# Kernel optimization log

Measured on AMD Instinct MI355X. Metric: run time of the kernel, lower is better.

The kernel has to match this reference:

```python
import jax, jax.numpy as jnp
import numpy as np

N, E, C, L, NG = 50000, 600000, 128, 7, 512
EPS = 1e-7


def layer_norm(z, g, b):
    mu = z.mean(-1, keepdims=True)
    var = ((z - mu) ** 2).mean(-1, keepdims=True)
    return (z - mu) * jax.lax.rsqrt(var + 1e-5) * g + b


def setup_inputs() -> dict:
    key = jax.random.key(0)
    ks = jax.random.split(key, 16)
    inp = {
        'x': jax.random.randint(ks[0], (N, 9), 0, 64, dtype=jnp.int32),
        'edge_index': jax.random.randint(ks[1], (2, E), 0, N, dtype=jnp.int32),
        'edge_attr': jax.random.randint(ks[2], (E, 3), 0, 8, dtype=jnp.int32),
        'batch': jnp.sort(jax.random.randint(ks[3], (N,), 0, NG, dtype=jnp.int32)),
        'atom_emb': jax.random.normal(ks[4], (9, 64, C), jnp.float32) * 0.1,
        'bond_emb': jax.random.normal(ks[5], (3, 8, C), jnp.float32) * 0.1,
        'vn_emb': jnp.zeros((1, C), jnp.float32),
        'conv_W1': jax.random.normal(ks[6], (L, C, 2 * C), jnp.float32) / np.sqrt(C),
        'conv_b1': jnp.zeros((L, 2 * C), jnp.float32),
        'conv_g1': jnp.ones((L, 2 * C), jnp.float32),
        'conv_bb1': jnp.zeros((L, 2 * C), jnp.float32),
        'conv_W2': jax.random.normal(ks[7], (L, 2 * C, C), jnp.float32) / np.sqrt(2 * C),
        'conv_b2': jnp.zeros((L, C), jnp.float32),
        'norm_g': jnp.ones((L, C), jnp.float32),
        'norm_b': jnp.zeros((L, C), jnp.float32),
        'vn_W1': jax.random.normal(ks[8], (L - 1, C, C), jnp.float32) / np.sqrt(C),
        'vn_b1': jnp.zeros((L - 1, C), jnp.float32),
        'vn_g': jnp.ones((L - 1, C), jnp.float32),
        'vn_bb': jnp.zeros((L - 1, C), jnp.float32),
        'vn_W2': jax.random.normal(ks[9], (L - 1, C, C), jnp.float32) / np.sqrt(C),
        'vn_b2': jnp.zeros((L - 1, C), jnp.float32),
    }
    return inp


def reference(x, edge_index, edge_attr, batch, atom_emb, bond_emb, vn_emb,
              conv_W1, conv_b1, conv_g1, conv_bb1, conv_W2, conv_b2,
              norm_g, norm_b, vn_W1, vn_b1, vn_g, vn_bb, vn_W2, vn_b2):
    src, dst = edge_index[0], edge_index[1]

    # AtomEncoder: sum of per-feature embeddings -> [N, C]
    h = atom_emb[jnp.arange(9), x].sum(axis=1)
    # BondEncoder (conv_encode_edge=False) -> [E, C]
    edge_emb = bond_emb[jnp.arange(3), edge_attr].sum(axis=1)

    # virtual node embedding (one per graph)
    vn = jnp.broadcast_to(vn_emb[0], (NG, C))
    h = h + vn[batch]

    def gen_conv(l, hx):
        # GENConv: msg = relu(x_j + e) + eps; softmax aggregation (t=1); MLP(x+m)
        msg = jax.nn.relu(hx[src] + edge_emb) + EPS                      # [E, C]
        mx = jax.ops.segment_max(msg, dst, num_segments=N)               # [N, C]
        e = jnp.exp(msg - mx[dst])
        den = jax.ops.segment_sum(e, dst, num_segments=N)
        m = jax.ops.segment_sum(msg * (e / (den[dst] + 1e-16)), dst, num_segments=N)
        z = hx + m
        z = jax.nn.relu(layer_norm(z @ conv_W1[l] + conv_b1[l], conv_g1[l], conv_bb1[l]))
        return z @ conv_W2[l] + conv_b2[l]

    # res+ block: Conv -> [Norm -> ReLU -> (VN update) -> Conv + res]*
    h = gen_conv(0, h)
    for l in range(1, L):
        h2 = jax.nn.relu(layer_norm(h, norm_g[l - 1], norm_b[l - 1]))
        vtmp = jax.ops.segment_sum(h2, batch, num_segments=NG) + vn
        v = jax.nn.relu(layer_norm(vtmp @ vn_W1[l - 1] + vn_b1[l - 1], vn_g[l - 1], vn_bb[l - 1]))
        vn = v @ vn_W2[l - 1] + vn_b2[l - 1]
        h2 = h2 + vn[batch]
        h = gen_conv(l, h2) + h
    h = layer_norm(h, norm_g[L - 1], norm_b[L - 1])

    # global_add_pool -> [NG, C]
    return jax.ops.segment_sum(h, batch, num_segments=NG)
```

## Files before the change

kernel.cpp:

```cpp
#include <hip/hip_runtime.h>
#include <hip/hip_bf16.h>
#include <stdint.h>

#define N_NODES 50000
#define N_EDGES 600000
#define CH 128
#define NLAYERS 7
#define NGRAPHS 512

typedef __hip_bfloat16 bf16;
using bf16x8 = __attribute__((ext_vector_type(8))) __bf16;
using f32x4  = __attribute__((ext_vector_type(4))) float;
using u32x4  = __attribute__((ext_vector_type(4))) uint32_t;

static __device__ __forceinline__ float b2f(bf16 v){ return __bfloat162float(v); }

static __device__ __forceinline__ void bar_lds(){
  asm volatile("s_waitcnt lgkmcnt(0)" ::: "memory");
  __builtin_amdgcn_sched_barrier(0);
  __builtin_amdgcn_s_barrier();
}

__global__ void k_detect(const uint32_t* __restrict__ g, int* __restrict__ flag){
  if (threadIdx.x == 0 && blockIdx.x == 0) flag[0] = (g[0] == 0x3F803F80u) ? 1 : 0;
}

struct Segs { const void* src[12]; float* dst[12]; int n[12]; };

__global__ void k_cvt_all(const int* __restrict__ flag, Segs S){
  int f = flag[0];
  int seg = blockIdx.y;
  int n = S.n[seg];
  const void* src = S.src[seg];
  float* dst = S.dst[seg];
  for (int i = blockIdx.x*blockDim.x + threadIdx.x; i < n; i += gridDim.x*blockDim.x)
    dst[i] = f ? b2f(((const bf16*)src)[i]) : ((const float*)src)[i];
}

__global__ void k_transpose_all(const int* __restrict__ flag,
    const void* W1, const void* W2, const void* vW1, const void* vW2,
    bf16* W1p, bf16* W2T, bf16* vW1p, bf16* vW2T){
  int f = flag[0];
  const int T0 = NLAYERS*128*256, T1 = NLAYERS*256*128;
  const int T2 = (NLAYERS-1)*128*128;
  int total = T0+T1+2*T2;
  for (int i = blockIdx.x*blockDim.x + threadIdx.x; i < total; i += gridDim.x*blockDim.x){
    float v;
    if (i < T0){
      int idx = i; int l = idx/(128*256); int rem = idx - l*128*256; int k = rem >> 8; int n = rem & 255;
      v = f ? b2f(((const bf16*)W1)[idx]) : ((const float*)W1)[idx];
      W1p[(size_t)l*256*128 + n*128 + (k ^ ((n&7)<<3))] = __float2bfloat16(v);
    } else if (i < T0+T1){
      int idx = i-T0; int l = idx/(256*128); int rem = idx - l*256*128; int k = rem >> 7; int n = rem & 127;
      v = f ? b2f(((const bf16*)W2)[idx]) : ((const float*)W2)[idx];
      W2T[(size_t)l*128*256 + n*256 + k] = __float2bfloat16(v);
    } else if (i < T0+T1+T2){
      int idx = i-T0-T1; int l = idx/(128*128); int rem = idx - l*128*128; int k = rem >> 7; int n = rem & 127;
      v = f ? b2f(((const bf16*)vW1)[idx]) : ((const float*)vW1)[idx];
      vW1p[(size_t)l*128*128 + n*128 + (k ^ ((n&7)<<3))] = __float2bfloat16(v);
    } else {
      int idx = i-T0-T1-T2; int l = idx/(128*128); int rem = idx - l*128*128; int k = rem >> 7; int n = rem & 127;
      v = f ? b2f(((const bf16*)vW2)[idx]) : ((const float*)vW2)[idx];
      vW2T[(size_t)l*128*128 + n*128 + k] = __float2bfloat16(v);
    }
  }
}

__global__ void k_bondC(const int* __restrict__ flag, const void* __restrict__ bond,
                        float* __restrict__ bondC){
  int f = flag[0];
  int i = blockIdx.x*blockDim.x + threadIdx.x;
  if (i >= 512*128) return;
  int idx = i >> 7, c = i & 127;
  int a0 = idx & 7, a1 = (idx>>3) & 7, a2 = (idx>>6) & 7;
  auto g = [&](int e)->float{ return f ? b2f(((const bf16*)bond)[e]) : ((const float*)bond)[e]; };
  bondC[i] = g((0*8+a0)*128 + c) + g((1*8+a1)*128 + c) + g((2*8+a2)*128 + c);
}

__global__ void k_zero_i32(int* p, int n){
  for (int i = blockIdx.x*blockDim.x + threadIdx.x; i < n; i += gridDim.x*blockDim.x) p[i] = 0;
}

__global__ void k_hist(const int* __restrict__ keys, int* __restrict__ counts, int n){
  for (int i = blockIdx.x*blockDim.x + threadIdx.x; i < n; i += gridDim.x*blockDim.x)
    atomicAdd(&counts[keys[i]], 1);
}

__global__ __launch_bounds__(256) void k_scanA(const int* __restrict__ in, int* __restrict__ out,
                                               int* __restrict__ bsums, int n){
  __shared__ int lds[256];
  int t = threadIdx.x;
  int base = blockIdx.x * 1024;
  int v[4]; int s = 0;
  #pragma unroll
  for (int i=0;i<4;i++){ int idx = base + t*4 + i; int x = (idx<n)? in[idx] : 0; v[i]=x; s+=x; }
  lds[t] = s; __syncthreads();
  for (int off=1; off<256; off<<=1){
    int x = (t>=off)? lds[t-off] : 0;
    __syncthreads();
    lds[t] += x;
    __syncthreads();
  }
  int p = lds[t] - s;
  #pragma unroll
  for (int i=0;i<4;i++){ int idx = base + t*4 + i; if (idx<n) out[idx] = p; p += v[i]; }
  if (t==255) bsums[blockIdx.x] = lds[255];
}

__global__ __launch_bounds__(256) void k_scanB(int* bsums, int nblk){
  __shared__ int lds[256];
  int t = threadIdx.x;
  int v = (t<nblk)? bsums[t] : 0;
  lds[t] = v; __syncthreads();
  for (int off=1; off<256; off<<=1){
    int x = (t>=off)? lds[t-off] : 0;
    __syncthreads();
    lds[t] += x;
    __syncthreads();
  }
  if (t<nblk) bsums[t] = lds[t] - v;
}

__global__ void k_scanC(int* out, const int* bsums, int n){
  for (int i = blockIdx.x*blockDim.x + threadIdx.x; i < n; i += gridDim.x*blockDim.x)
    out[i] += bsums[i >> 10];
}

__global__ void k_scatter(const int* __restrict__ ei, const int* __restrict__ ea,
                          const int* __restrict__ row_ptr, int* __restrict__ fill,
                          uint32_t* __restrict__ csr){
  for (int e = blockIdx.x*blockDim.x + threadIdx.x; e < N_EDGES; e += gridDim.x*blockDim.x){
    int src = ei[e];
    int dst = ei[N_EDGES + e];
    int pos = row_ptr[dst] + atomicAdd(&fill[dst], 1);
    uint32_t a0 = (uint32_t)ea[e*3+0], a1 = (uint32_t)ea[e*3+1], a2 = (uint32_t)ea[e*3+2];
    csr[pos] = (uint32_t)src | ((a0 | (a1<<3) | (a2<<6)) << 16);
  }
}

__global__ void k_gptr(const int* __restrict__ batch, int* __restrict__ gptr){
  int i = blockIdx.x*blockDim.x + threadIdx.x;
  if (i >= N_NODES) return;
  int b = batch[i];
  if (i == 0){ for (int g=0; g<=b; ++g) gptr[g] = 0; }
  else { int bp = batch[i-1]; for (int g=bp+1; g<=b; ++g) gptr[g] = i; }
  if (i == N_NODES-1){ for (int g=b+1; g<=NGRAPHS; ++g) gptr[g] = N_NODES; }
}

__global__ __launch_bounds__(128) void k_atom_encode(const int* __restrict__ x,
    const float* __restrict__ atom_emb, const float* __restrict__ vn_emb,
    uint32_t* __restrict__ hxb){
  int n = blockIdx.x; int c = threadIdx.x;
  float s = vn_emb[c];
  #pragma unroll
  for (int f=0; f<9; ++f){
    int xv = x[n*9+f];
    s += atom_emb[(f*64 + xv)*CH + c];
  }
  float o = __shfl_xor(s, 1);
  if ((c & 1) == 0){
    __hip_bfloat162 p; p.x = __float2bfloat16(s); p.y = __float2bfloat16(o);
    hxb[n*64 + (c>>1)] = *reinterpret_cast<uint32_t*>(&p);
  }
}

__global__ void k_vn_init(const float* __restrict__ vn_emb, float* __restrict__ vn){
  for (int i = blockIdx.x*blockDim.x + threadIdx.x; i < NGRAPHS*CH; i += gridDim.x*blockDim.x)
    vn[i] = vn_emb[i & (CH-1)];
}

__global__ __launch_bounds__(64) void k_aggregate(const uint32_t* __restrict__ hxb,
     const uint32_t* __restrict__ csr, const int* __restrict__ row_ptr,
     const float* __restrict__ bondC, uint32_t* __restrict__ z){
  int n = blockIdx.x; int t = threadIdx.x;
  int s0 = row_ptr[n], s1 = row_ptr[n+1];
  float sa=0.f, sb=0.f, wa=0.f, wb=0.f;
  int i = s0;
  for (; i+4 <= s1; i += 4){
    uint32_t u0=csr[i], u1=csr[i+1], u2=csr[i+2], u3=csr[i+3];
    uint32_t h0 = hxb[(size_t)(u0 & 0xFFFFu)*64 + t];
    uint32_t h1 = hxb[(size_t)(u1 & 0xFFFFu)*64 + t];
    uint32_t h2 = hxb[(size_t)(u2 & 0xFFFFu)*64 + t];
    uint32_t h3 = hxb[(size_t)(u3 & 0xFFFFu)*64 + t];
    float2 c0 = *reinterpret_cast<const float2*>(bondC + (size_t)(u0 >> 16)*128 + 2*t);
    float2 c1 = *reinterpret_cast<const float2*>(bondC + (size_t)(u1 >> 16)*128 + 2*t);
    float2 c2 = *reinterpret_cast<const float2*>(bondC + (size_t)(u2 >> 16)*128 + 2*t);
    float2 c3 = *reinterpret_cast<const float2*>(bondC + (size_t)(u3 >> 16)*128 + 2*t);
    #define EDGE(hp, bc) { \
      float va = __uint_as_float(hp << 16) + bc.x; \
      float vb = __uint_as_float(hp & 0xFFFF0000u) + bc.y; \
      va = fmaxf(va, 0.f) + 1e-7f; vb = fmaxf(vb, 0.f) + 1e-7f; \
      float pa = __expf(va - 10.f), pb = __expf(vb - 10.f); \
      sa += pa; wa += pa*va; sb += pb; wb += pb*vb; }
    EDGE(h0, c0) EDGE(h1, c1) EDGE(h2, c2) EDGE(h3, c3)
  }
  for (; i < s1; ++i){
    uint32_t u = csr[i];
    uint32_t hp = hxb[(size_t)(u & 0xFFFFu)*64 + t];
    float2 bc = *reinterpret_cast<const float2*>(bondC + (size_t)(u >> 16)*128 + 2*t);
    EDGE(hp, bc)
    #undef EDGE
  }
  uint32_t own = hxb[(size_t)n*64 + t];
  float za = __uint_as_float(own << 16)         + wa/(sa + 1e-16f);
  float zb = __uint_as_float(own & 0xFFFF0000u) + wb/(sb + 1e-16f);
  __hip_bfloat162 p; p.x = __float2bfloat16(za); p.y = __float2bfloat16(zb);
  z[(size_t)n*64 + (t ^ ((n&7)<<2))] = *reinterpret_cast<uint32_t*>(&p);
}

template<int K, int N1, int N2, bool VNIN>
__global__ __launch_bounds__(512, 2) void k_mlp7(const bf16* __restrict__ A,
    const float* __restrict__ Af32,
    const bf16* __restrict__ W1s,
    const float* __restrict__ b1, const float* __restrict__ g1, const float* __restrict__ bb1,
    const bf16* __restrict__ W2T,
    const float* __restrict__ b2,
    const float* __restrict__ lng, const float* __restrict__ lnb,
    const float* __restrict__ residual, float* __restrict__ out,
    float* __restrict__ hxout, int relu2, int M, int NT)
{
  constexpr int KK1 = K/32;
  constexpr int WC  = N1/4;
  constexpr int JC  = WC/16;
  constexpr int KK2 = N1/32;
  __shared__ __align__(16) bf16 W1L[N1*K];
  __shared__ __align__(16) bf16 AL[2][64*K];
  __shared__ __align__(16) bf16 zt[64*N1];
  __shared__ float lnp[64][4][2];
  __shared__ float lnv[64][2];

  const int tid = threadIdx.x;
  const int wid = tid >> 6, lane = tid & 63;
  const int wr = wid >> 2, wc = wid & 3;
  const int rlo = lane & 15, hi = lane >> 4, khi = hi*8;

  {
    constexpr int NC_ = (N1*K*2)/1024/8;
    #pragma unroll
    for (int c=0;c<NC_;++c){
      int cc = c*8 + wid;
      __builtin_amdgcn_global_load_lds((const uint32_t*)((const char*)W1s + cc*1024 + lane*16),
                                       (uint32_t*)((char*)W1L + cc*1024), 16, 0, 0);
    }
  }

  float b1v[JC], gv[JC], bbv[JC];
  #pragma unroll
  for (int jc=0;jc<JC;++jc){
    int col = wc*WC + jc*16 + rlo;
    b1v[jc] = b1[col]; gv[jc] = g1[col]; bbv[jc] = bb1[col];
  }
  float bv2[2] = { b2[wc*32 + rlo], b2[wc*32 + 16 + rlo] };
  float lngv[2] = {0.f,0.f}, lnbv[2] = {0.f,0.f};
  if (hxout){
    lngv[0] = lng[wc*32 + rlo];      lnbv[0] = lnb[wc*32 + rlo];
    lngv[1] = lng[wc*32 + 16 + rlo]; lnbv[1] = lnb[wc*32 + 16 + rlo];
  }
  u32x4 b2raw[2][KK2];
  #pragma unroll
  for (int ct=0;ct<2;++ct){
    const bf16* wp = W2T + (size_t)(wc*32 + ct*16 + rlo)*N1 + khi;
    #pragma unroll
    for (int kk=0;kk<KK2;++kk){
      b2raw[ct][kk] = *reinterpret_cast<const u32x4*>(wp + kk*32);
      asm volatile("" : "+v"(b2raw[ct][kk]));
    }
  }

  auto stageA = [&](int nb, int tile){
    if constexpr (!VNIN){
      const char* src = (const char*)A + (size_t)tile*(64*K*2);
      constexpr int NCA = (64*K*2)/1024/8;
      #pragma unroll
      for (int c=0;c<NCA;++c){
        int cc = c*8 + wid;
        __builtin_amdgcn_global_load_lds((const uint32_t*)(src + cc*1024 + lane*16),
                                         (uint32_t*)((char*)&AL[nb][0] + cc*1024), 16, 0, 0);
      }
    } else {
      int base = tile*64;
      #pragma unroll
      for (int e=0;e<(64*K/4)/512;++e){
        int idx = tid + e*512;
        int row = idx >> 5;
        int k4  = (idx & 31)*4;
        float4 v = *reinterpret_cast<const float4*>(Af32 + (size_t)(base+row)*K + k4);
        int s = (row&7)<<3;
        bf16* d = &AL[nb][row*K + (k4 ^ s)];
        d[0]=__float2bfloat16(v.x); d[1]=__float2bfloat16(v.y);
        d[2]=__float2bfloat16(v.z); d[3]=__float2bfloat16(v.w);
      }
    }
  };

  int t = blockIdx.x, buf = 0;
  stageA(0, t);
  __syncthreads();

  while (true){
    int tn = t + (int)gridDim.x;

    f32x4 acc1[2][JC];
    #pragma unroll
    for (int rt=0;rt<2;++rt)
      #pragma unroll
      for (int jc=0;jc<JC;++jc) acc1[rt][jc] = {0.f,0.f,0.f,0.f};
    #pragma unroll
    for (int kk=0;kk<KK1;++kk){
      bf16x8 af[2], bw[JC];
      #pragma unroll
      for (int rt=0;rt<2;++rt){
        int lr = wr*32 + rt*16 + rlo;
        af[rt] = *reinterpret_cast<const bf16x8*>(&AL[buf][lr*K + ((kk*32 + khi) ^ ((lr&7)<<3))]);
      }
      #pragma unroll
      for (int jc=0;jc<JC;++jc){
        int n = wc*WC + jc*16 + rlo;
        bw[jc] = *reinterpret_cast<const bf16x8*>(&W1L[n*K + ((kk*32 + khi) ^ ((n&7)<<3))]);
      }
      #pragma unroll
      for (int rt=0;rt<2;++rt)
        #pragma unroll
        for (int jc=0;jc<JC;++jc)
          acc1[rt][jc] = __builtin_amdgcn_mfma_f32_16x16x32_bf16(af[rt], bw[jc], acc1[rt][jc], 0,0,0);
    }

    if (tn < NT) stageA(buf^1, tn);
    float resv[2][2][4];
    if (residual){
      #pragma unroll
      for (int rt=0;rt<2;++rt)
        #pragma unroll
        for (int r=0;r<4;++r){
          int grow = t*64 + wr*32 + rt*16 + hi*4 + r; if (grow >= M) grow = M-1;
          #pragma unroll
          for (int ct=0;ct<2;++ct)
            resv[rt][ct][r] = residual[(size_t)grow*N2 + wc*32 + ct*16 + rlo];
        }
    }
    __builtin_amdgcn_sched_barrier(0);

    float p[2][4], q[2][4];
    #pragma unroll
    for (int rt=0;rt<2;++rt)
      #pragma unroll
      for (int r=0;r<4;++r){ p[rt][r]=0.f; q[rt][r]=0.f; }
    #pragma unroll
    for (int jc=0;jc<JC;++jc)
      #pragma unroll
      for (int rt=0;rt<2;++rt)
        #pragma unroll
        for (int r=0;r<4;++r){
          float v = acc1[rt][jc][r] + b1v[jc]; acc1[rt][jc][r] = v;
          p[rt][r] += v; q[rt][r] += v*v;
        }
    #pragma unroll
    for (int rt=0;rt<2;++rt)
      #pragma unroll
      for (int r=0;r<4;++r){
        float pv = p[rt][r], qv = q[rt][r];
        #pragma unroll
        for (int off=1; off<16; off<<=1){ pv += __shfl_xor(pv, off); qv += __shfl_xor(qv, off); }
        if (rlo == 0){
          int row = wr*32 + rt*16 + hi*4 + r;
          lnp[row][wc][0] = pv; lnp[row][wc][1] = qv;
        }
      }
    bar_lds();
    if (tid < 64){
      float P=0.f, Q=0.f;
      #pragma unroll
      for (int w=0;w<4;++w){ P += lnp[tid][w][0]; Q += lnp[tid][w][1]; }
      float mu = P*(1.f/N1);
      lnv[tid][0] = mu;
      lnv[tid][1] = rsqrtf(Q*(1.f/N1) - mu*mu + 1e-5f);
    }
    bar_lds();

    #pragma unroll
    for (int rt=0;rt<2;++rt)
      #pragma unroll
      for (int r=0;r<4;++r){
        int row = wr*32 + rt*16 + hi*4 + r;
        float mu = lnv[row][0], rs = lnv[row][1];
        #pragma unroll
        for (int jc=0;jc<JC;++jc){
          int col = wc*WC + jc*16 + rlo;
          float y = (acc1[rt][jc][r]-mu)*rs*gv[jc] + bbv[jc];
          zt[row*N1 + (col ^ ((row&7)<<3))] = __float2bfloat16(fmaxf(y, 0.f));
        }
      }
    bar_lds();

    f32x4 acc2[2][2];
    #pragma unroll
    for (int rt=0;rt<2;++rt)
      #pragma unroll
      for (int ct=0;ct<2;++ct) acc2[rt][ct] = {0.f,0.f,0.f,0.f};
    #pragma unroll
    for (int kk=0;kk<KK2;++kk){
      bf16x8 a2[2];
      #pragma unroll
      for (int rt=0;rt<2;++rt){
        int row = wr*32 + rt*16 + rlo;
        a2[rt] = *reinterpret_cast<const bf16x8*>(&zt[row*N1 + ((kk*32 + khi) ^ ((row&7)<<3))]);
      }
      #pragma unroll
      for (int rt=0;rt<2;++rt)
        #pragma unroll
        for (int ct=0;ct<2;++ct){
          bf16x8 bb;
          __builtin_memcpy(&bb, &b2raw[ct][kk], 16);
          acc2[rt][ct] = __builtin_amdgcn_mfma_f32_16x16x32_bf16(a2[rt], bb, acc2[rt][ct], 0,0,0);
        }
    }

    float vmat[2][2][4];
    #pragma unroll
    for (int rt=0;rt<2;++rt)
      #pragma unroll
      for (int ct=0;ct<2;++ct)
        #pragma unroll
        for (int r=0;r<4;++r){
          float v = acc2[rt][ct][r] + bv2[ct];
          if (residual) v += resv[rt][ct][r];
          vmat[rt][ct][r] = v;
          int grow = t*64 + wr*32 + rt*16 + hi*4 + r;
          if (grow < M) out[(size_t)grow*N2 + wc*32 + ct*16 + rlo] = v;
        }

    if (hxout){
      #pragma unroll
      for (int rt=0;rt<2;++rt)
        #pragma unroll
        for (int r=0;r<4;++r){
          float pv = vmat[rt][0][r] + vmat[rt][1][r];
          float qv = vmat[rt][0][r]*vmat[rt][0][r] + vmat[rt][1][r]*vmat[rt][1][r];
          #pragma unroll
          for (int off=1; off<16; off<<=1){ pv += __shfl_xor(pv, off); qv += __shfl_xor(qv, off); }
          if (rlo == 0){
            int row = wr*32 + rt*16 + hi*4 + r;
            lnp[row][wc][0] = pv; lnp[row][wc][1] = qv;
          }
        }
      bar_lds();
      if (tid < 64){
        float P=0.f, Q=0.f;
        #pragma unroll
        for (int w=0;w<4;++w){ P += lnp[tid][w][0]; Q += lnp[tid][w][1]; }
        float mu = P*(1.f/N2);
        lnv[tid][0] = mu;
        lnv[tid][1] = rsqrtf(Q*(1.f/N2) - mu*mu + 1e-5f);
      }
      bar_lds();
      #pragma unroll
      for (int rt=0;rt<2;++rt)
        #pragma unroll
        for (int r=0;r<4;++r){
          int row = wr*32 + rt*16 + hi*4 + r;
          float mu = lnv[row][0], rs = lnv[row][1];
          int grow = t*64 + row;
          if (grow < M){
            #pragma unroll
            for (int ct=0;ct<2;++ct){
              float y = (vmat[rt][ct][r]-mu)*rs*lngv[ct] + lnbv[ct];
              if (relu2) y = fmaxf(y, 0.f);
              hxout[(size_t)grow*N2 + wc*32 + ct*16 + rlo] = y;
            }
          }
        }
    }

    if (tn >= NT) break;
    t = tn; buf ^= 1;
    __syncthreads();
  }
}

__global__ void k_vncopy(const float* __restrict__ vn, float* __restrict__ vnacc){
  int i = blockIdx.x*blockDim.x + threadIdx.x;
  if (i < NGRAPHS*CH) vnacc[i] = vn[i];
}

#define SEGC 128
__global__ __launch_bounds__(128) void k_segsum2(const float* __restrict__ hx,
    const int* __restrict__ batch, float* __restrict__ vnacc){
  int c = threadIdx.x;
  int n0 = blockIdx.x*SEGC;
  int n1 = n0 + SEGC; if (n1 > N_NODES) n1 = N_NODES;
  if (n0 >= N_NODES) return;
  int cur = batch[n0];
  float s = 0.f;
  for (int n = n0; n < n1; ++n){
    int b = batch[n];
    if (b != cur){ atomicAdd(&vnacc[cur*CH + c], s); s = 0.f; cur = b; }
    s += hx[(size_t)n*CH + c];
  }
  atomicAdd(&vnacc[cur*CH + c], s);
}

__global__ void k_add_vn(const float* __restrict__ hx, const float* __restrict__ vn,
                         const int* __restrict__ batch, uint32_t* __restrict__ hxb){
  for (int i = blockIdx.x*blockDim.x + threadIdx.x; i < N_NODES*64; i += gridDim.x*blockDim.x){
    int n = i >> 6; int t = i & 63;
    float2 hv = *reinterpret_cast<const float2*>(hx + (size_t)n*CH + 2*t);
    float2 vv = *reinterpret_cast<const float2*>(vn + (size_t)batch[n]*CH + 2*t);
    __hip_bfloat162 p; p.x = __float2bfloat16(hv.x+vv.x); p.y = __float2bfloat16(hv.y+vv.y);
    hxb[i] = *reinterpret_cast<uint32_t*>(&p);
  }
}

__global__ __launch_bounds__(128) void k_pool(const float* __restrict__ hx,
    const int* __restrict__ gptr, const int* __restrict__ flag, void* __restrict__ out){
  int g = blockIdx.x; int c = threadIdx.x;
  float s = 0.f;
  for (int n = gptr[g]; n < gptr[g+1]; ++n) s += hx[(size_t)n*CH + c];
  if (flag[0]) ((bf16*)out)[g*CH+c] = __float2bfloat16(s);
  else         ((float*)out)[g*CH+c] = s;
}

extern "C" void kernel_launch(void* const* d_in, const int* in_sizes, int n_in,
                              void* d_out, int out_size, void* d_ws, size_t ws_size,
                              hipStream_t stream)
{
  const int*  x     = (const int*) d_in[0];
  const int*  ei    = (const int*) d_in[1];
  const int*  ea    = (const int*) d_in[2];
  const int*  batch = (const int*) d_in[3];
  const void* atom_emb = d_in[4];
  const void* bond_emb = d_in[5];
  const void* vn_emb   = d_in[6];
  const void* conv_W1  = d_in[7];
  const void* conv_b1  = d_in[8];
  const void* conv_g1  = d_in[9];
  const void* conv_bb1 = d_in[10];
  const void* conv_W2  = d_in[11];
  const void* conv_b2  = d_in[12];
  const void* norm_g   = d_in[13];
  const void* norm_b   = d_in[14];
  const void* vn_W1    = d_in[15];
  const void* vn_b1    = d_in[16];
  const void* vn_g     = d_in[17];
  const void* vn_bb    = d_in[18];
  const void* vn_W2    = d_in[19];
  const void* vn_b2    = d_in[20];

  char* wsb = (char*)d_ws;
  size_t off = 0;
  auto alloc = [&](size_t bytes)->char*{ char* p = wsb + off; off += (bytes + 255) & ~(size_t)255; return p; };
  const int ZROWS = 50048;
  float*    h     = (float*)   alloc(sizeof(float)*N_NODES*CH);
  float*    hx    = (float*)   alloc(sizeof(float)*N_NODES*CH);
  uint32_t* hxb   = (uint32_t*)alloc(sizeof(uint32_t)*N_NODES*64);
  uint32_t* z     = (uint32_t*)alloc(sizeof(uint32_t)*ZROWS*64);
  float*    vn    = (float*)   alloc(sizeof(float)*NGRAPHS*CH);
  float*    vnacc = (float*)   alloc(sizeof(float)*NGRAPHS*CH);
  bf16*     W1Tp  = (bf16*)    alloc(sizeof(bf16)*NLAYERS*256*128);
  bf16*     W2T   = (bf16*)    alloc(sizeof(bf16)*NLAYERS*128*256);
  bf16*     vW1Tp = (bf16*)    alloc(sizeof(bf16)*(NLAYERS-1)*128*128);
  bf16*     vW2T  = (bf16*)    alloc(sizeof(bf16)*(NLAYERS-1)*128*128);
  int* row_ptr = (int*)alloc(sizeof(int)*(N_NODES+1));
  int* counts  = (int*)alloc(sizeof(int)*(N_NODES+1));
  uint32_t* csr = (uint32_t*)alloc(sizeof(uint32_t)*N_EDGES);
  int* gptr    = (int*)alloc(sizeof(int)*(NGRAPHS+1));
  int* bsums   = (int*)alloc(sizeof(int)*256);
  int* flag    = (int*)alloc(sizeof(int)*64);
  float* atomF = (float*)alloc(sizeof(float)*9*64*CH);
  float* bondC = (float*)alloc(sizeof(float)*512*CH);
  float* vnEF  = (float*)alloc(sizeof(float)*CH);
  float* b1F   = (float*)alloc(sizeof(float)*NLAYERS*2*CH);
  float* g1F   = (float*)alloc(sizeof(float)*NLAYERS*2*CH);
  float* bb1F  = (float*)alloc(sizeof(float)*NLAYERS*2*CH);
  float* b2F   = (float*)alloc(sizeof(float)*NLAYERS*CH);
  float* ngF   = (float*)alloc(sizeof(float)*NLAYERS*CH);
  float* nbF   = (float*)alloc(sizeof(float)*NLAYERS*CH);
  float* vb1F  = (float*)alloc(sizeof(float)*(NLAYERS-1)*CH);
  float* vgF   = (float*)alloc(sizeof(float)*(NLAYERS-1)*CH);
  float* vbbF  = (float*)alloc(sizeof(float)*(NLAYERS-1)*CH);
  float* vb2F  = (float*)alloc(sizeof(float)*(NLAYERS-1)*CH);

  k_detect<<<1, 64, 0, stream>>>((const uint32_t*)norm_g, flag);
  Segs S;
  int si = 0;
  auto seg = [&](const void* s_, float* d_, int n_){ S.src[si]=s_; S.dst[si]=d_; S.n[si]=n_; ++si; };
  seg(atom_emb, atomF, 9*64*CH);
  seg(vn_emb,   vnEF,  CH);
  seg(conv_b1,  b1F,  NLAYERS*2*CH);
  seg(conv_g1,  g1F,  NLAYERS*2*CH);
  seg(conv_bb1, bb1F, NLAYERS*2*CH);
  seg(conv_b2,  b2F,  NLAYERS*CH);
  seg(norm_g,   ngF,  NLAYERS*CH);
  seg(norm_b,   nbF,  NLAYERS*CH);
  seg(vn_b1,    vb1F, (NLAYERS-1)*CH);
  seg(vn_g,     vgF,  (NLAYERS-1)*CH);
  seg(vn_bb,    vbbF, (NLAYERS-1)*CH);
  seg(vn_b2,    vb2F, (NLAYERS-1)*CH);
  k_cvt_all<<<dim3(72, 12), 256, 0, stream>>>(flag, S);
  k_transpose_all<<<640, 256, 0, stream>>>(flag, conv_W1, conv_W2, vn_W1, vn_W2,
                                           W1Tp, W2T, vW1Tp, vW2T);
  k_bondC<<<256, 256, 0, stream>>>(flag, bond_emb, bondC);

  k_zero_i32<<<64, 256, 0, stream>>>(counts, N_NODES+1);
  k_hist<<<512, 256, 0, stream>>>(ei + N_EDGES, counts, N_EDGES);
  int nblkE = (N_NODES+1 + 1023)/1024;
  k_scanA<<<nblkE, 256, 0, stream>>>(counts, row_ptr, bsums, N_NODES+1);
  k_scanB<<<1, 256, 0, stream>>>(bsums, nblkE);
  k_scanC<<<64, 256, 0, stream>>>(row_ptr, bsums, N_NODES+1);
  k_zero_i32<<<64, 256, 0, stream>>>(counts, N_NODES+1);
  k_scatter<<<512, 256, 0, stream>>>(ei, ea, row_ptr, counts, csr);
  k_gptr<<<(N_NODES+255)/256, 256, 0, stream>>>(batch, gptr);

  k_atom_encode<<<N_NODES, 128, 0, stream>>>(x, atomF, vnEF, hxb);
  k_vn_init<<<64, 256, 0, stream>>>(vnEF, vn);

  const int NT_CONV = (N_NODES + 63)/64;
  const int NT_VN   = NGRAPHS/64;

  for (int l = 0; l < NLAYERS; ++l){
    if (l > 0){
      k_vncopy<<<(NGRAPHS*CH+255)/256, 256, 0, stream>>>(vn, vnacc);
      k_segsum2<<<(N_NODES+SEGC-1)/SEGC, 128, 0, stream>>>(hx, batch, vnacc);
      k_mlp7<128,128,128,true><<<NT_VN, 512, 0, stream>>>(nullptr, vnacc,
          vW1Tp + (size_t)(l-1)*128*128, vb1F + (l-1)*CH, vgF + (l-1)*CH, vbbF + (l-1)*CH,
          vW2T + (size_t)(l-1)*128*128, vb2F + (l-1)*CH,
          nullptr, nullptr, nullptr, vn, nullptr, 0, NGRAPHS, NT_VN);
      k_add_vn<<<1024, 256, 0, stream>>>(hx, vn, batch, hxb);
    }
    k_aggregate<<<N_NODES, 64, 0, stream>>>(hxb, csr, row_ptr, bondC, z);
    k_mlp7<128,256,128,false><<<256, 512, 0, stream>>>((const bf16*)z, nullptr,
        W1Tp + (size_t)l*256*128, b1F + l*2*CH, g1F + l*2*CH, bb1F + l*2*CH,
        W2T + (size_t)l*128*256, b2F + l*CH,
        ngF + l*CH, nbF + l*CH,
        (l==0)? nullptr : h, h, hx, (l < NLAYERS-1) ? 1 : 0, N_NODES, NT_CONV);
  }
  k_pool<<<NGRAPHS, 128, 0, stream>>>(hx, gptr, flag, d_out);
}
```

Baseline: 965.8 us.

## Hold W1 in registers, drop persistent loop, and store normalized activations as bf16

The MLP kernel stops staging W1 into LDS. Each wave now holds its W1 slice in VGPRs, which frees LDS and lets launch bounds rise to 4 blocks per CU with one tile per block instead of a persistent double-buffered loop. The normalized activation hx is now written as bf16 instead of fp32, which halves traffic in the segsum, add_vn and pool kernels. The costs are heavier register pressure, which may cause spills at the higher occupancy target, the loss of the prefetch overlap, and lower precision in the pooled and VN sums.

After: 1.257 ms. 1.3x slower.

```diff
diff --git a/kernel.cpp b/kernel.cpp
--- a/kernel.cpp
+++ b/kernel.cpp
@@ -49,7 +49,7 @@
     if (i < T0){
       int idx = i; int l = idx/(128*256); int rem = idx - l*128*256; int k = rem >> 8; int n = rem & 255;
       v = f ? b2f(((const bf16*)W1)[idx]) : ((const float*)W1)[idx];
-      W1p[(size_t)l*256*128 + n*128 + (k ^ ((n&7)<<3))] = __float2bfloat16(v);
+      W1p[(size_t)l*256*128 + n*128 + k] = __float2bfloat16(v);
     } else if (i < T0+T1){
       int idx = i-T0; int l = idx/(256*128); int rem = idx - l*256*128; int k = rem >> 7; int n = rem & 127;
       v = f ? b2f(((const bf16*)W2)[idx]) : ((const float*)W2)[idx];
@@ -57,7 +57,7 @@
     } else if (i < T0+T1+T2){
       int idx = i-T0-T1; int l = idx/(128*128); int rem = idx - l*128*128; int k = rem >> 7; int n = rem & 127;
       v = f ? b2f(((const bf16*)vW1)[idx]) : ((const float*)vW1)[idx];
-      vW1p[(size_t)l*128*128 + n*128 + (k ^ ((n&7)<<3))] = __float2bfloat16(v);
+      vW1p[(size_t)l*128*128 + n*128 + k] = __float2bfloat16(v);
     } else {
       int idx = i-T0-T1-T2; int l = idx/(128*128); int rem = idx - l*128*128; int k = rem >> 7; int n = rem & 127;
       v = f ? b2f(((const bf16*)vW2)[idx]) : ((const float*)vW2)[idx];
@@ -209,22 +209,21 @@
 }
 
 template<int K, int N1, int N2, bool VNIN>
-__global__ __launch_bounds__(512, 2) void k_mlp7(const bf16* __restrict__ A,
+__global__ __launch_bounds__(512, 4) void k_mlp8(const bf16* __restrict__ A,
     const float* __restrict__ Af32,
-    const bf16* __restrict__ W1s,
+    const bf16* __restrict__ W1T,
     const float* __restrict__ b1, const float* __restrict__ g1, const float* __restrict__ bb1,
     const bf16* __restrict__ W2T,
     const float* __restrict__ b2,
     const float* __restrict__ lng, const float* __restrict__ lnb,
     const float* __restrict__ residual, float* __restrict__ out,
-    float* __restrict__ hxout, int relu2, int M, int NT)
+    bf16* __restrict__ hxn, int relu2, int M)
 {
   constexpr int KK1 = K/32;
   constexpr int WC  = N1/4;
   constexpr int JC  = WC/16;
   constexpr int KK2 = N1/32;
-  __shared__ __align__(16) bf16 W1L[N1*K];
-  __shared__ __align__(16) bf16 AL[2][64*K];
+  __shared__ __align__(16) bf16 AL[64*K];
   __shared__ __align__(16) bf16 zt[64*N1];
   __shared__ float lnp[64][4][2];
   __shared__ float lnv[64][2];
@@ -233,14 +232,39 @@
   const int wid = tid >> 6, lane = tid & 63;
   const int wr = wid >> 2, wc = wid & 3;
   const int rlo = lane & 15, hi = lane >> 4, khi = hi*8;
-
-  {
-    constexpr int NC_ = (N1*K*2)/1024/8;
-    #pragma unroll
-    for (int c=0;c<NC_;++c){
+  const int t = blockIdx.x;
+
+  u32x4 w1raw[JC][KK1];
+  #pragma unroll
+  for (int jc=0;jc<JC;++jc){
+    const bf16* wp = W1T + (size_t)(wc*WC + jc*16 + rlo)*K + khi;
+    #pragma unroll
+    for (int kk=0;kk<KK1;++kk){
+      w1raw[jc][kk] = *reinterpret_cast<const u32x4*>(wp + kk*32);
+      asm volatile("" : "+v"(w1raw[jc][kk]));
+    }
+  }
+
+  if constexpr (!VNIN){
+    const char* src = (const char*)A + (size_t)t*(64*K*2);
+    #pragma unroll
+    for (int c=0;c<2;++c){
       int cc = c*8 + wid;
-      __builtin_amdgcn_global_load_lds((const uint32_t*)((const char*)W1s + cc*1024 + lane*16),
-                                       (uint32_t*)((char*)W1L + cc*1024), 16, 0, 0);
+      __builtin_amdgcn_global_load_lds((const uint32_t*)(src + cc*1024 + lane*16),
+                                       (uint32_t*)((char*)AL + cc*1024), 16, 0, 0);
+    }
+  } else {
+    int base = t*64;
+    #pragma unroll
+    for (int e=0;e<(64*K/4)/512;++e){
+      int idx = tid + e*512;
+      int row = idx >> 5;
+      int k4  = (idx & 31)*4;
+      float4 v = *reinterpret_cast<const float4*>(Af32 + (size_t)(base+row)*K + k4);
+      int s = (row&7)<<3;
+      bf16* d = &AL[row*K + (k4 ^ s)];
+      d[0]=__float2bfloat16(v.x); d[1]=__float2bfloat16(v.y);
+      d[2]=__float2bfloat16(v.z); d[3]=__float2bfloat16(v.w);
     }
   }
 
@@ -252,10 +276,35 @@
   }
   float bv2[2] = { b2[wc*32 + rlo], b2[wc*32 + 16 + rlo] };
   float lngv[2] = {0.f,0.f}, lnbv[2] = {0.f,0.f};
-  if (hxout){
+  if (hxn){
     lngv[0] = lng[wc*32 + rlo];      lnbv[0] = lnb[wc*32 + rlo];
     lngv[1] = lng[wc*32 + 16 + rlo]; lnbv[1] = lnb[wc*32 + 16 + rlo];
   }
+  __syncthreads();
+
+  f32x4 acc1[2][JC];
+  #pragma unroll
+  for (int rt=0;rt<2;++rt)
+    #pragma unroll
+    for (int jc=0;jc<JC;++jc) acc1[rt][jc] = {0.f,0.f,0.f,0.f};
+  #pragma unroll
+  for (int kk=0;kk<KK1;++kk){
+    bf16x8 af[2];
+    #pragma unroll
+    for (int rt=0;rt<2;++rt){
+      int lr = wr*32 + rt*16 + rlo;
+      af[rt] = *reinterpret_cast<const bf16x8*>(&AL[lr*K + ((kk*32 + khi) ^ ((lr&7)<<3))]);
+    }
+    #pragma unroll
+    for (int rt=0;rt<2;++rt)
+      #pragma unroll
+      for (int jc=0;jc<JC;++jc){
+        bf16x8 bw;
+        __builtin_memcpy(&bw, &w1raw[jc][kk], 16);
+        acc1[rt][jc] = __builtin_amdgcn_mfma_f32_16x16x32_bf16(af[rt], bw, acc1[rt][jc], 0,0,0);
+      }
+  }
+
   u32x4 b2raw[2][KK2];
   #pragma unroll
   for (int ct=0;ct<2;++ct){
@@ -266,99 +315,116 @@
       asm volatile("" : "+v"(b2raw[ct][kk]));
     }
   }
-
-  auto stageA = [&](int nb, int tile){
-    if constexpr (!VNIN){
-      const char* src = (const char*)A + (size_t)tile*(64*K*2);
-      constexpr int NCA = (64*K*2)/1024/8;
-      #pragma unroll
-      for (int c=0;c<NCA;++c){
-        int cc = c*8 + wid;
-        __builtin_amdgcn_global_load_lds((const uint32_t*)(src + cc*1024 + lane*16),
-                                         (uint32_t*)((char*)&AL[nb][0] + cc*1024), 16, 0, 0);
-      }
-    } else {
-      int base = tile*64;
-      #pragma unroll
-      for (int e=0;e<(64*K/4)/512;++e){
-        int idx = tid + e*512;
-        int row = idx >> 5;
-        int k4  = (idx & 31)*4;
-        float4 v = *reinterpret_cast<const float4*>(Af32 + (size_t)(base+row)*K + k4);
-        int s = (row&7)<<3;
-        bf16* d = &AL[nb][row*K + (k4 ^ s)];
-        d[0]=__float2bfloat16(v.x); d[1]=__float2bfloat16(v.y);
-        d[2]=__float2bfloat16(v.z); d[3]=__float2bfloat16(v.w);
-      }
-    }
-  };
-
-  int t = blockIdx.x, buf = 0;
-  stageA(0, t);
-  __syncthreads();
-
-  while (true){
-    int tn = t + (int)gridDim.x;
-
-    f32x4 acc1[2][JC];
+  float resv[2][2][4];
+  if (residual){
     #pragma unroll
     for (int rt=0;rt<2;++rt)
       #pragma unroll
-      for (int jc=0;jc<JC;++jc) acc1[rt][jc] = {0.f,0.f,0.f,0.f};
-    #pragma unroll
-    for (int kk=0;kk<KK1;++kk){
-      bf16x8 af[2], bw[JC];
-      #pragma unroll
-      for (int rt=0;rt<2;++rt){
-        int lr = wr*32 + rt*16 + rlo;
-        af[rt] = *reinterpret_cast<const bf16x8*>(&AL[buf][lr*K + ((kk*32 + khi) ^ ((lr&7)<<3))]);
-      }
+      for (int r=0;r<4;++r){
+        int grow = t*64 + wr*32 + rt*16 + hi*4 + r; if (grow >= M) grow = M-1;
+        #pragma unroll
+        for (int ct=0;ct<2;++ct)
+          resv[rt][ct][r] = residual[(size_t)grow*N2 + wc*32 + ct*16 + rlo];
+      }
+  }
+  __builtin_amdgcn_sched_barrier(0);
+
+  float p[2][4], q[2][4];
+  #pragma unroll
+  for (int rt=0;rt<2;++rt)
+    #pragma unroll
+    for (int r=0;r<4;++r){ p[rt][r]=0.f; q[rt][r]=0.f; }
+  #pragma unroll
+  for (int jc=0;jc<JC;++jc)
+    #pragma unroll
+    for (int rt=0;rt<2;++rt)
+      #pragma unroll
+      for (int r=0;r<4;++r){
+        float v = acc1[rt][jc][r] + b1v[jc]; acc1[rt][jc][r] = v;
+        p[rt][r] += v; q[rt][r] += v*v;
+      }
+  #pragma unroll
+  for (int rt=0;rt<2;++rt)
+    #pragma unroll
+    for (int r=0;r<4;++r){
+      float pv = p[rt][r], qv = q[rt][r];
+      #pragma unroll
+      for (int off=1; off<16; off<<=1){ pv += __shfl_xor(pv, off); qv += __shfl_xor(qv, off); }
+      if (rlo == 0){
+        int row = wr*32 + rt*16 + hi*4 + r;
+        lnp[row][wc][0] = pv; lnp[row][wc][1] = qv;
+      }
+    }
+  bar_lds();
+  if (tid < 64){
+    float P=0.f, Q=0.f;
+    #pragma unroll
+    for (int w=0;w<4;++w){ P += lnp[tid][w][0]; Q += lnp[tid][w][1]; }
+    float mu = P*(1.f/N1);
+    lnv[tid][0] = mu;
+    lnv[tid][1] = rsqrtf(Q*(1.f/N1) - mu*mu + 1e-5f);
+  }
+  bar_lds();
+
+  #pragma unroll
+  for (int rt=0;rt<2;++rt)
+    #pragma unroll
+    for (int r=0;r<4;++r){
+      int row = wr*32 + rt*16 + hi*4 + r;
+      float mu = lnv[row][0], rs = lnv[row][1];
       #pragma unroll
       for (int jc=0;jc<JC;++jc){
-        int n = wc*WC + jc*16 + rlo;
-        bw[jc] = *reinterpret_cast<const bf16x8*>(&W1L[n*K + ((kk*32 + khi) ^ ((n&7)<<3))]);
-      }
-      #pragma unroll
-      for (int rt=0;rt<2;++rt)
-        #pragma unroll
-        for (int jc=0;jc<JC;++jc)
-          acc1[rt][jc] = __builtin_amdgcn_mfma_f32_16x16x32_bf16(af[rt], bw[jc], acc1[rt][jc], 0,0,0);
-    }
-
-    if (tn < NT) stageA(buf^1, tn);
-    float resv[2][2][4];
-    if (residual){
-      #pragma unroll
-      for (int rt=0;rt<2;++rt)
-        #pragma unroll
-        for (int r=0;r<4;++r){
-          int grow = t*64 + wr*32 + rt*16 + hi*4 + r; if (grow >= M) grow = M-1;
-          #pragma unroll
-          for (int ct=0;ct<2;++ct)
-            resv[rt][ct][r] = residual[(size_t)grow*N2 + wc*32 + ct*16 + rlo];
-        }
-    }
-    __builtin_amdgcn_sched_barrier(0);
-
-    float p[2][4], q[2][4];
+        int col = wc*WC + jc*16 + rlo;
+        float y = (acc1[rt][jc][r]-mu)*rs*gv[jc] + bbv[jc];
+        zt[row*N1 + (col ^ ((row&7)<<3))] = __float2bfloat16(fmaxf(y, 0.f));
+      }
+    }
+  bar_lds();
+
+  f32x4 acc2[2][2];
+  #pragma unroll
+  for (int rt=0;rt<2;++rt)
+    #pragma unroll
+    for (int ct=0;ct<2;++ct) acc2[rt][ct] = {0.f,0.f,0.f,0.f};
+  #pragma unroll
+  for (int kk=0;kk<KK2;++kk){
+    bf16x8 a2[2];
+    #pragma unroll
+    for (int rt=0;rt<2;++rt){
+      int row = wr*32 + rt*16 + rlo;
+      a2[rt] = *reinterpret_cast<const bf16x8*>(&zt[row*N1 + ((kk*32 + khi) ^ ((row&7)<<3))]);
+    }
     #pragma unroll
     for (int rt=0;rt<2;++rt)
       #pragma unroll
-      for (int r=0;r<4;++r){ p[rt][r]=0.f; q[rt][r]=0.f; }
-    #pragma unroll
-    for (int jc=0;jc<JC;++jc)
-      #pragma unroll
-      for (int rt=0;rt<2;++rt)
-        #pragma unroll
-        for (int r=0;r<4;++r){
-          float v = acc1[rt][jc][r] + b1v[jc]; acc1[rt][jc][r] = v;
-          p[rt][r] += v; q[rt][r] += v*v;
-        }
+      for (int ct=0;ct<2;++ct){
+        bf16x8 bb;
+        __builtin_memcpy(&bb, &b2raw[ct][kk], 16);
+        acc2[rt][ct] = __builtin_amdgcn_mfma_f32_16x16x32_bf16(a2[rt], bb, acc2[rt][ct], 0,0,0);
+      }
+  }
+
+  float vmat[2][2][4];
+  #pragma unroll
+  for (int rt=0;rt<2;++rt)
+    #pragma unroll
+    for (int ct=0;ct<2;++ct)
+      #pragma unroll
+      for (int r=0;r<4;++r){
+        float v = acc2[rt][ct][r] + bv2[ct];
+        if (residual) v += resv[rt][ct][r];
+        vmat[rt][ct][r] = v;
+        int grow = t*64 + wr*32 + rt*16 + hi*4 + r;
+        if (grow < M) out[(size_t)grow*N2 + wc*32 + ct*16 + rlo] = v;
+      }
+
+  if (hxn){
     #pragma unroll
     for (int rt=0;rt<2;++rt)
       #pragma unroll
       for (int r=0;r<4;++r){
-        float pv = p[rt][r], qv = q[rt][r];
+        float pv = vmat[rt][0][r] + vmat[rt][1][r];
+        float qv = vmat[rt][0][r]*vmat[rt][0][r] + vmat[rt][1][r]*vmat[rt][1][r];
         #pragma unroll
         for (int off=1; off<16; off<<=1){ pv += __shfl_xor(pv, off); qv += __shfl_xor(qv, off); }
         if (rlo == 0){
@@ -371,109 +437,27 @@
       float P=0.f, Q=0.f;
       #pragma unroll
       for (int w=0;w<4;++w){ P += lnp[tid][w][0]; Q += lnp[tid][w][1]; }
-      float mu = P*(1.f/N1);
+      float mu = P*(1.f/N2);
       lnv[tid][0] = mu;
-      lnv[tid][1] = rsqrtf(Q*(1.f/N1) - mu*mu + 1e-5f);
+      lnv[tid][1] = rsqrtf(Q*(1.f/N2) - mu*mu + 1e-5f);
     }
     bar_lds();
-
     #pragma unroll
     for (int rt=0;rt<2;++rt)
       #pragma unroll
       for (int r=0;r<4;++r){
         int row = wr*32 + rt*16 + hi*4 + r;
         float mu = lnv[row][0], rs = lnv[row][1];
-        #pragma unroll
-        for (int jc=0;jc<JC;++jc){
-          int col = wc*WC + jc*16 + rlo;
-          float y = (acc1[rt][jc][r]-mu)*rs*gv[jc] + bbv[jc];
-          zt[row*N1 + (col ^ ((row&7)<<3))] = __float2bfloat16(fmaxf(y, 0.f));
-        }
-      }
-    bar_lds();
-
-    f32x4 acc2[2][2];
-    #pragma unroll
-    for (int rt=0;rt<2;++rt)
-      #pragma unroll
-      for (int ct=0;ct<2;++ct) acc2[rt][ct] = {0.f,0.f,0.f,0.f};
-    #pragma unroll
-    for (int kk=0;kk<KK2;++kk){
-      bf16x8 a2[2];
-      #pragma unroll
-      for (int rt=0;rt<2;++rt){
-        int row = wr*32 + rt*16 + rlo;
-        a2[rt] = *reinterpret_cast<const bf16x8*>(&zt[row*N1 + ((kk*32 + khi) ^ ((row&7)<<3))]);
-      }
-      #pragma unroll
-      for (int rt=0;rt<2;++rt)
-        #pragma unroll
-        for (int ct=0;ct<2;++ct){
-          bf16x8 bb;
-          __builtin_memcpy(&bb, &b2raw[ct][kk], 16);
-          acc2[rt][ct] = __builtin_amdgcn_mfma_f32_16x16x32_bf16(a2[rt], bb, acc2[rt][ct], 0,0,0);
-        }
-    }
-
-    float vmat[2][2][4];
-    #pragma unroll
-    for (int rt=0;rt<2;++rt)
-      #pragma unroll
-      for (int ct=0;ct<2;++ct)
-        #pragma unroll
-        for (int r=0;r<4;++r){
-          float v = acc2[rt][ct][r] + bv2[ct];
-          if (residual) v += resv[rt][ct][r];
-          vmat[rt][ct][r] = v;
-          int grow = t*64 + wr*32 + rt*16 + hi*4 + r;
-          if (grow < M) out[(size_t)grow*N2 + wc*32 + ct*16 + rlo] = v;
-        }
-
-    if (hxout){
-      #pragma unroll
-      for (int rt=0;rt<2;++rt)
-        #pragma unroll
-        for (int r=0;r<4;++r){
-          float pv = vmat[rt][0][r] + vmat[rt][1][r];
-          float qv = vmat[rt][0][r]*vmat[rt][0][r] + vmat[rt][1][r]*vmat[rt][1][r];
+        int grow = t*64 + row;
+        if (grow < M){
           #pragma unroll
-          for (int off=1; off<16; off<<=1){ pv += __shfl_xor(pv, off); qv += __shfl_xor(qv, off); }
-          if (rlo == 0){
-            int row = wr*32 + rt*16 + hi*4 + r;
-            lnp[row][wc][0] = pv; lnp[row][wc][1] = qv;
+          for (int ct=0;ct<2;++ct){
+            float y = (vmat[rt][ct][r]-mu)*rs*lngv[ct] + lnbv[ct];
+            if (relu2) y = fmaxf(y, 0.f);
+            hxn[(size_t)grow*N2 + wc*32 + ct*16 + rlo] = __float2bfloat16(y);
           }
         }
-      bar_lds();
-      if (tid < 64){
-        float P=0.f, Q=0.f;
-        #pragma unroll
-        for (int w=0;w<4;++w){ P += lnp[tid][w][0]; Q += lnp[tid][w][1]; }
-        float mu = P*(1.f/N2);
-        lnv[tid][0] = mu;
-        lnv[tid][1] = rsqrtf(Q*(1.f/N2) - mu*mu + 1e-5f);
-      }
-      bar_lds();
-      #pragma unroll
-      for (int rt=0;rt<2;++rt)
-        #pragma unroll
-        for (int r=0;r<4;++r){
-          int row = wr*32 + rt*16 + hi*4 + r;
-          float mu = lnv[row][0], rs = lnv[row][1];
-          int grow = t*64 + row;
-          if (grow < M){
-            #pragma unroll
-            for (int ct=0;ct<2;++ct){
-              float y = (vmat[rt][ct][r]-mu)*rs*lngv[ct] + lnbv[ct];
-              if (relu2) y = fmaxf(y, 0.f);
-              hxout[(size_t)grow*N2 + wc*32 + ct*16 + rlo] = y;
-            }
-          }
-        }
-    }
-
-    if (tn >= NT) break;
-    t = tn; buf ^= 1;
-    __syncthreads();
+      }
   }
 }
 
@@ -483,7 +467,7 @@
 }
 
 #define SEGC 128
-__global__ __launch_bounds__(128) void k_segsum2(const float* __restrict__ hx,
+__global__ __launch_bounds__(128) void k_segsum2(const bf16* __restrict__ hxn,
     const int* __restrict__ batch, float* __restrict__ vnacc){
   int c = threadIdx.x;
   int n0 = blockIdx.x*SEGC;
@@ -494,27 +478,29 @@
   for (int n = n0; n < n1; ++n){
     int b = batch[n];
     if (b != cur){ atomicAdd(&vnacc[cur*CH + c], s); s = 0.f; cur = b; }
-    s += hx[(size_t)n*CH + c];
+    s += b2f(hxn[(size_t)n*CH + c]);
   }
   atomicAdd(&vnacc[cur*CH + c], s);
 }
 
-__global__ void k_add_vn(const float* __restrict__ hx, const float* __restrict__ vn,
+__global__ void k_add_vn(const uint32_t* __restrict__ hxn, const float* __restrict__ vn,
                          const int* __restrict__ batch, uint32_t* __restrict__ hxb){
   for (int i = blockIdx.x*blockDim.x + threadIdx.x; i < N_NODES*64; i += gridDim.x*blockDim.x){
     int n = i >> 6; int t = i & 63;
-    float2 hv = *reinterpret_cast<const float2*>(hx + (size_t)n*CH + 2*t);
+    uint32_t hp = hxn[i];
     float2 vv = *reinterpret_cast<const float2*>(vn + (size_t)batch[n]*CH + 2*t);
-    __hip_bfloat162 p; p.x = __float2bfloat16(hv.x+vv.x); p.y = __float2bfloat16(hv.y+vv.y);
+    float za = __uint_as_float(hp << 16)         + vv.x;
+    float zb = __uint_as_float(hp & 0xFFFF0000u) + vv.y;
+    __hip_bfloat162 p; p.x = __float2bfloat16(za); p.y = __float2bfloat16(zb);
     hxb[i] = *reinterpret_cast<uint32_t*>(&p);
   }
 }
 
-__global__ __launch_bounds__(128) void k_pool(const float* __restrict__ hx,
+__global__ __launch_bounds__(128) void k_pool(const bf16* __restrict__ hxn,
     const int* __restrict__ gptr, const int* __restrict__ flag, void* __restrict__ out){
   int g = blockIdx.x; int c = threadIdx.x;
   float s = 0.f;
-  for (int n = gptr[g]; n < gptr[g+1]; ++n) s += hx[(size_t)n*CH + c];
+  for (int n = gptr[g]; n < gptr[g+1]; ++n) s += b2f(hxn[(size_t)n*CH + c]);
   if (flag[0]) ((bf16*)out)[g*CH+c] = __float2bfloat16(s);
   else         ((float*)out)[g*CH+c] = s;
 }
@@ -550,14 +536,14 @@
   auto alloc = [&](size_t bytes)->char*{ char* p = wsb + off; off += (bytes + 255) & ~(size_t)255; return p; };
   const int ZROWS = 50048;
   float*    h     = (float*)   alloc(sizeof(float)*N_NODES*CH);
-  float*    hx    = (float*)   alloc(sizeof(float)*N_NODES*CH);
+  uint32_t* hxn   = (uint32_t*)alloc(sizeof(uint32_t)*ZROWS*64);
   uint32_t* hxb   = (uint32_t*)alloc(sizeof(uint32_t)*N_NODES*64);
   uint32_t* z     = (uint32_t*)alloc(sizeof(uint32_t)*ZROWS*64);
   float*    vn    = (float*)   alloc(sizeof(float)*NGRAPHS*CH);
   float*    vnacc = (float*)   alloc(sizeof(float)*NGRAPHS*CH);
-  bf16*     W1Tp  = (bf16*)    alloc(sizeof(bf16)*NLAYERS*256*128);
+  bf16*     W1Tl  = (bf16*)    alloc(sizeof(bf16)*NLAYERS*256*128);
   bf16*     W2T   = (bf16*)    alloc(sizeof(bf16)*NLAYERS*128*256);
-  bf16*     vW1Tp = (bf16*)    alloc(sizeof(bf16)*(NLAYERS-1)*128*128);
+  bf16*     vW1Tl = (bf16*)    alloc(sizeof(bf16)*(NLAYERS-1)*128*128);
   bf16*     vW2T  = (bf16*)    alloc(sizeof(bf16)*(NLAYERS-1)*128*128);
   int* row_ptr = (int*)alloc(sizeof(int)*(N_NODES+1));
   int* counts  = (int*)alloc(sizeof(int)*(N_NODES+1));
@@ -597,7 +583,7 @@
   seg(vn_b2,    vb2F, (NLAYERS-1)*CH);
   k_cvt_all<<<dim3(72, 12), 256, 0, stream>>>(flag, S);
   k_transpose_all<<<640, 256, 0, stream>>>(flag, conv_W1, conv_W2, vn_W1, vn_W2,
-                                           W1Tp, W2T, vW1Tp, vW2T);
+                                           W1Tl, W2T, vW1Tl, vW2T);
   k_bondC<<<256, 256, 0, stream>>>(flag, bond_emb, bondC);
 
   k_zero_i32<<<64, 256, 0, stream>>>(counts, N_NODES+1);
@@ -619,19 +605,19 @@
   for (int l = 0; l < NLAYERS; ++l){
     if (l > 0){
       k_vncopy<<<(NGRAPHS*CH+255)/256, 256, 0, stream>>>(vn, vnacc);
-      k_segsum2<<<(N_NODES+SEGC-1)/SEGC, 128, 0, stream>>>(hx, batch, vnacc);
-      k_mlp7<128,128,128,true><<<NT_VN, 512, 0, stream>>>(nullptr, vnacc,
-          vW1Tp + (size_t)(l-1)*128*128, vb1F + (l-1)*CH, vgF + (l-1)*CH, vbbF + (l-1)*CH,
+      k_segsum2<<<(N_NODES+SEGC-1)/SEGC, 128, 0, stream>>>((const bf16*)hxn, batch, vnacc);
+      k_mlp8<128,128,128,true><<<NT_VN, 512, 0, stream>>>(nullptr, vnacc,
+          vW1Tl + (size_t)(l-1)*128*128, vb1F + (l-1)*CH, vgF + (l-1)*CH, vbbF + (l-1)*CH,
           vW2T + (size_t)(l-1)*128*128, vb2F + (l-1)*CH,
-          nullptr, nullptr, nullptr, vn, nullptr, 0, NGRAPHS, NT_VN);
-      k_add_vn<<<1024, 256, 0, stream>>>(hx, vn, batch, hxb);
+          nullptr, nullptr, nullptr, vn, nullptr, 0, NGRAPHS);
+      k_add_vn<<<1024, 256, 0, stream>>>(hxn, vn, batch, hxb);
     }
     k_aggregate<<<N_NODES, 64, 0, stream>>>(hxb, csr, row_ptr, bondC, z);
-    k_mlp7<128,256,128,false><<<256, 512, 0, stream>>>((const bf16*)z, nullptr,
-        W1Tp + (size_t)l*256*128, b1F + l*2*CH, g1F + l*2*CH, bb1F + l*2*CH,
+    k_mlp8<128,256,128,false><<<NT_CONV, 512, 0, stream>>>((const bf16*)z, nullptr,
+        W1Tl + (size_t)l*256*128, b1F + l*2*CH, g1F + l*2*CH, bb1F + l*2*CH,
         W2T + (size_t)l*128*256, b2F + l*CH,
         ngF + l*CH, nbF + l*CH,
-        (l==0)? nullptr : h, h, hx, (l < NLAYERS-1) ? 1 : 0, N_NODES, NT_CONV);
-  }
-  k_pool<<<NGRAPHS, 128, 0, stream>>>(hx, gptr, flag, d_out);
-}
+        (l==0)? nullptr : h, h, (bf16*)hxn, (l < NLAYERS-1) ? 1 : 0, N_NODES);
+  }
+  k_pool<<<NGRAPHS, 128, 0, stream>>>((const bf16*)hxn, gptr, flag, d_out);
+}
```
